# Performance work log

Measured on AMD Instinct MI355X. Metric: run time of the kernel, lower is better.

## Reference

```python
import jax, jax.numpy as jnp
import numpy as np

WS = 7          # window size
NH = 8          # num heads
EPS = 1e-5


def _rel_pos_index(ws):
    # timm WindowAttention relative_position_index, shape (ws*ws, ws*ws), values in [0, (2ws-1)^2)
    coords = np.stack(np.meshgrid(np.arange(ws), np.arange(ws), indexing='ij'))  # 2,ws,ws
    coords = coords.reshape(2, -1)
    rel = coords[:, :, None] - coords[:, None, :]          # 2,N,N
    rel = rel.transpose(1, 2, 0)                           # N,N,2
    rel[:, :, 0] += ws - 1
    rel[:, :, 1] += ws - 1
    rel[:, :, 0] *= 2 * ws - 1
    return rel.sum(-1)                                     # N,N

RPI = jnp.asarray(_rel_pos_index(WS), dtype=jnp.int32)


def _ln(x, g, b):
    mu = jnp.mean(x, axis=-1, keepdims=True)
    var = jnp.mean(jnp.square(x - mu), axis=-1, keepdims=True)
    return (x - mu) * jax.lax.rsqrt(var + EPS) * g + b


def setup_inputs() -> dict:
    key = jax.random.key(0)
    ks = jax.random.split(key, 16)
    C, Hd, V = 256, 1024, 7
    s = lambda k, shp, fan: jax.random.normal(k, shp, jnp.float32) * (fan ** -0.5)
    return {
        'x': jax.random.normal(ks[0], (256, 256, 14, 14), jnp.float32),
        'conv_w': s(ks[1], (C, C), C), 'conv_b': jnp.zeros((C,), jnp.float32),
        'ln1_g': jnp.ones((C,), jnp.float32), 'ln1_b': jnp.zeros((C,), jnp.float32),
        'qkv_w': s(ks[2], (C, 3 * C), C), 'qkv_b': jnp.zeros((3 * C,), jnp.float32),
        'rpb': 0.02 * jax.random.normal(ks[3], ((2 * WS - 1) ** 2, NH), jnp.float32),
        'proj_w': s(ks[4], (C, C), C), 'proj_b': jnp.zeros((C,), jnp.float32),
        'ln2_g': jnp.ones((C,), jnp.float32), 'ln2_b': jnp.zeros((C,), jnp.float32),
        'fc1_w': s(ks[5], (C, Hd), C), 'fc1_b': jnp.zeros((Hd,), jnp.float32),
        'fc2_w': s(ks[6], (Hd, C), Hd), 'fc2_b': jnp.zeros((C,), jnp.float32),
        'fc_out_w': s(ks[7], (C, V), C), 'fc_out_b': jnp.zeros((V,), jnp.float32),
    }


def reference(x, conv_w, conv_b, ln1_g, ln1_b, qkv_w, qkv_b, rpb, proj_w, proj_b,
              ln2_g, ln2_b, fc1_w, fc1_b, fc2_w, fc2_b, fc_out_w, fc_out_b):
    B, Cin, H, W = x.shape
    C = conv_w.shape[0]
    hd = C // NH
    # 1x1 conv projection -> tokens (B, H*W, C)
    t = jnp.einsum('oc,bchw->bhwo', conv_w, x) + conv_b            # B,H,W,C
    tok = t.reshape(B, H * W, C)
    # --- Swin block, shift_size=0 ---
    shortcut = tok
    y = _ln(tok, ln1_g, ln1_b).reshape(B, H, W, C)
    # window partition -> (B*nW, ws*ws, C)
    nHw, nWw = H // WS, W // WS
    yw = y.reshape(B, nHw, WS, nWw, WS, C).transpose(0, 1, 3, 2, 4, 5)
    yw = yw.reshape(B * nHw * nWw, WS * WS, C)
    N = WS * WS
    qkv = (yw @ qkv_w + qkv_b).reshape(-1, N, 3, NH, hd).transpose(2, 0, 3, 1, 4)
    q, k, v = qkv[0], qkv[1], qkv[2]                               # (Bn, NH, N, hd)
    attn = jnp.einsum('bhqd,bhkd->bhqk', q * (hd ** -0.5), k)
    attn = attn + rpb[RPI].transpose(2, 0, 1)[None]                # + (NH,N,N) bias
    attn = jax.nn.softmax(attn, axis=-1)
    o = jnp.einsum('bhqk,bhkd->bqhd', attn, v).reshape(-1, N, C)
    o = o @ proj_w + proj_b
    # window reverse
    o = o.reshape(B, nHw, nWw, WS, WS, C).transpose(0, 1, 3, 2, 4, 5).reshape(B, H * W, C)
    tok = shortcut + o                                             # drop_path = identity (eval)
    h = _ln(tok, ln2_g, ln2_b)
    h = jax.nn.gelu(h @ fc1_w + fc1_b, approximate=False) @ fc2_w + fc2_b
    tok = tok + h
    # global average pool over spatial tokens, then classifier
    pooled = jnp.mean(tok, axis=1)                                 # B,C
    return pooled @ fc_out_w + fc_out_b
```

## Files before the change

kernel.cpp:

```cpp
#include <hip/hip_runtime.h>
#include <math.h>

#define NHEADS 8
#define BATCH  256
#define HWTOK  196
#define MTOT   50176

#define BM 128
#define BN 128
#define BK 64

typedef short bfrag8 __attribute__((ext_vector_type(8)));
typedef float ffrag4 __attribute__((ext_vector_type(4)));

__device__ __forceinline__ unsigned short f2bf(float f) {
  union { float f; unsigned u; } v; v.f = f;
  unsigned r = v.u + 0x7fffu + ((v.u >> 16) & 1u);
  return (unsigned short)(r >> 16);
}
__device__ __forceinline__ float bf2f(unsigned short b) {
  union { unsigned u; float f; } v; v.u = ((unsigned)b) << 16;
  return v.f;
}
__device__ __forceinline__ float bflo(unsigned u) {
  union { unsigned x; float f; } v; v.x = u << 16; return v.f;
}
__device__ __forceinline__ float bfhi(unsigned u) {
  union { unsigned x; float f; } v; v.x = u & 0xffff0000u; return v.f;
}
__device__ __forceinline__ unsigned cvtpk(float a, float b) {
  unsigned r;
  asm("v_cvt_pk_bf16_f32 %0, %1, %2" : "=v"(r) : "v"(a), "v"(b));
  return r;
}
__device__ __forceinline__ float gelu_fast(float x) {
  float ax = fabsf(x);
  float z = ax * 0.70710678118654752f;
  float t = __builtin_amdgcn_rcpf(fmaf(z, 0.3275911f, 1.0f));
  float y = t * (0.254829592f +
            t * (-0.284496736f +
            t * (1.421413741f +
            t * (-1.453152027f +
            t * 1.061405429f))));
  float e2 = __expf(-z * z);
  float erfv = fmaf(-y, e2, 1.0f);
  return 0.5f * fmaf(ax, erfv, x);
}
__device__ __forceinline__ int window_reverse_row(int m) {
  int widx = m / 49, pos = m % 49;
  int b = widx >> 2, wh = (widx >> 1) & 1, ww = widx & 1;
  int i = pos / 7, j = pos % 7;
  return b * 196 + (wh * 7 + i) * 14 + (ww * 7 + j);
}

__device__ __forceinline__ void gload16(const void* g, void* l) {
  __builtin_amdgcn_global_load_lds(
      (const __attribute__((address_space(1))) void*)g,
      (__attribute__((address_space(3))) void*)l, 16, 0, 0);
}

__device__ __forceinline__ int xcd_swz() {
  if (gridDim.x & 7) return (int)blockIdx.x;
  return (int)((blockIdx.x & 7) * (gridDim.x >> 3) + (blockIdx.x >> 3));
}

template <int EPI>
__global__ __launch_bounds__(256) void k_gemm_mfma(const unsigned short* __restrict__ A,
                                                   const unsigned short* __restrict__ BT,
                                                   const float* __restrict__ bias,
                                                   void* __restrict__ Cout,
                                                   int rowbase, int N, int K, int nNt) {
  __shared__ __align__(128) unsigned short S[16384];
  const int t = threadIdx.x;
  const int lane = t & 63, w = t >> 6;
  const int wr = w >> 1, wc = w & 1;
  const int lb = xcd_swz();
  const int n_t = lb % nNt, m_t = lb / nNt;
  const int m0 = m_t * BM, n0 = n_t * BN;
  const int l15 = lane & 15;
  const int sw = (lane & 7) << 3;
  const int rA = lane >> 3;
  const int kin = (((lane & 7) ^ rA) << 3);
  ffrag4 acc[4][4] = {};

  for (int k0 = 0; k0 < K; k0 += BK) {
#pragma unroll
    for (int i = 0; i < 4; ++i) {
      const int seg = i * 4 + w;
      const int row = seg * 8 + rA;
      gload16(A + (size_t)(m0 + row) * K + k0 + kin, (char*)S + seg * 1024);
      gload16(BT + (size_t)(n0 + row) * K + k0 + kin, (char*)S + 16384 + seg * 1024);
    }
    __syncthreads();
#pragma unroll
    for (int kk = 0; kk < BK; kk += 32) {
      bfrag8 af[4], bfr[4];
      const int colA = (kk + (lane >> 4) * 8) ^ sw;
#pragma unroll
      for (int mi = 0; mi < 4; ++mi) {
        int row = wr * 64 + mi * 16 + l15;
        af[mi] = *(const bfrag8*)&S[row * BK + colA];
      }
#pragma unroll
      for (int ni = 0; ni < 4; ++ni) {
        int col = wc * 64 + ni * 16 + l15;
        bfr[ni] = *(const bfrag8*)&S[8192 + col * BK + colA];
      }
#pragma unroll
      for (int mi = 0; mi < 4; ++mi)
#pragma unroll
        for (int ni = 0; ni < 4; ++ni)
          acc[mi][ni] = __builtin_amdgcn_mfma_f32_16x16x32_bf16(af[mi], bfr[ni], acc[mi][ni], 0, 0, 0);
    }
    __syncthreads();
  }

  const int cr = (lane >> 4) * 4;
  const int cc = l15;
  float bv[4];
#pragma unroll
  for (int ni = 0; ni < 4; ++ni) bv[ni] = bias[n0 + wc * 64 + ni * 16 + cc];

  float* Sf = (float*)S;
#pragma unroll
  for (int pass = 0; pass < 2; ++pass) {
    if (wr == pass) {
#pragma unroll
      for (int mi = 0; mi < 4; ++mi) {
#pragma unroll
        for (int j = 0; j < 4; ++j) {
          const int mloc = mi * 16 + cr + j;
#pragma unroll
          for (int ni = 0; ni < 4; ++ni) {
            const int nl = wc * 64 + ni * 16 + cc;
            Sf[mloc * 128 + nl] = acc[mi][ni][j] + bv[ni];
          }
        }
      }
    }
    __syncthreads();
#pragma unroll
    for (int r = 0; r < 4; ++r) {
      const int flat = (r * 256 + t) * 8;
      const int ml = flat >> 7, nl = flat & 127;
      float4 a = *(const float4*)&Sf[flat];
      float4 b2 = *(const float4*)&Sf[flat + 4];
      uint4 o;
      if (EPI == 2 || EPI == 3) {
        const int gm = rowbase + m0 + pass * 64 + ml;
        const int row = (EPI == 2) ? window_reverse_row(gm) : gm;
        unsigned short* dst = (unsigned short*)Cout + (size_t)row * N + n0 + nl;
        uint4 old = *(const uint4*)dst;
        o.x = cvtpk(bflo(old.x) + a.x, bfhi(old.x) + a.y);
        o.y = cvtpk(bflo(old.y) + a.z, bfhi(old.y) + a.w);
        o.z = cvtpk(bflo(old.z) + b2.x, bfhi(old.z) + b2.y);
        o.w = cvtpk(bflo(old.w) + b2.z, bfhi(old.w) + b2.w);
        *(uint4*)dst = o;
      } else {
        o.x = cvtpk(a.x, a.y);  o.y = cvtpk(a.z, a.w);
        o.z = cvtpk(b2.x, b2.y); o.w = cvtpk(b2.z, b2.w);
        *(uint4*)((unsigned short*)Cout + (size_t)(m0 + pass * 64 + ml) * N + n0 + nl) = o;
      }
    }
    if (pass == 0) __syncthreads();
  }
}

__global__ __launch_bounds__(256, 1) void k_mlp(const unsigned short* __restrict__ A,
                                                const unsigned short* __restrict__ fc1T,
                                                const unsigned short* __restrict__ fc2T,
                                                const float* __restrict__ b1g,
                                                const float* __restrict__ b2g,
                                                unsigned short* __restrict__ tok,
                                                int rowbase) {
  __shared__ __align__(128) char S[131072];
  unsigned short* Al = (unsigned short*)S;
  unsigned short* Bl = (unsigned short*)(S + 65536);
  unsigned short* Cl = (unsigned short*)(S + 98304);

  const int t = threadIdx.x;
  const int lane = t & 63, w = t >> 6;
  const int wr = w >> 1, wc = w & 1;
  const int l15 = lane & 15, g = lane >> 4;
  const int key = lane & 7;
  const int cr = (lane >> 4) * 4, cc = l15;
  const int m0 = xcd_swz() * 128;

  ffrag4 acc2[4][8] = {};

#pragma unroll
  for (int i = 0; i < 16; ++i) {
    const int inst = i * 4 + w;
    const int r = inst * 2 + (lane >> 5);
    const int sg = ((lane & 31) ^ (r & 7)) << 3;
    gload16(A + (size_t)(m0 + r) * 256 + sg, (char*)Al + inst * 1024);
  }

  for (int hc = 0; hc < 8; ++hc) {
    float b1[4];
#pragma unroll
    for (int ni = 0; ni < 4; ++ni)
      b1[ni] = b1g[hc * 128 + wc * 64 + ni * 16 + cc];

    ffrag4 acch[4][4] = {};
#pragma unroll
    for (int p = 0; p < 2; ++p) {
      __syncthreads();
#pragma unroll
      for (int i = 0; i < 8; ++i) {
        const int inst = i * 4 + w;
        const int r = inst * 4 + (lane >> 4);
        const int sg = p * 128 + (((lane & 15) ^ (r & 7)) << 3);
        gload16(fc1T + (size_t)(hc * 128 + r) * 256 + sg, (char*)Bl + inst * 1024);
      }
      __syncthreads();
#pragma unroll
      for (int kk = 0; kk < 128; kk += 32) {
        bfrag8 af[4], bf[4];
        const int qA = ((p * 16 + (kk >> 3) + g) ^ key) << 3;
        const int qB = (((kk >> 3) + g) ^ key) << 3;
#pragma unroll
        for (int mi = 0; mi < 4; ++mi)
          af[mi] = *(const bfrag8*)&Al[(wr * 64 + mi * 16 + l15) * 256 + qA];
#pragma unroll
        for (int ni = 0; ni < 4; ++ni)
          bf[ni] = *(const bfrag8*)&Bl[(wc * 64 + ni * 16 + l15) * 128 + qB];
#pragma unroll
        for (int mi = 0; mi < 4; ++mi)
#pragma unroll
          for (int ni = 0; ni < 4; ++ni)
            acch[mi][ni] = __builtin_amdgcn_mfma_f32_16x16x32_bf16(af[mi], bf[ni], acch[mi][ni], 0, 0, 0);
      }
    }
    __syncthreads();

#pragma unroll
    for (int mi = 0; mi < 4; ++mi) {
#pragma unroll
      for (int j = 0; j < 4; ++j) {
        const int row = wr * 64 + mi * 16 + cr + j;
        const int k8 = (row & 7) << 3;
#pragma unroll
        for (int ni = 0; ni < 4; ++ni) {
          const int col = wc * 64 + ni * 16 + cc;
          Cl[row * 128 + (col ^ k8)] = f2bf(gelu_fast(acch[mi][ni][j] + b1[ni]));
        }
      }
    }

#pragma unroll
    for (int h = 0; h < 2; ++h) {
      if (h == 1) __syncthreads();
#pragma unroll
      for (int i = 0; i < 8; ++i) {
        const int inst = i * 4 + w;
        const int r = inst * 8 + (lane >> 3);
        const int sg = hc * 128 + h * 64 + (((lane & 7) ^ (r & 7)) << 3);
        gload16(fc2T + (size_t)r * 1024 + sg, (char*)Bl + inst * 1024);
      }
      __syncthreads();
#pragma unroll
      for (int kk2 = 0; kk2 < 64; kk2 += 32) {
        bfrag8 af2[4], bf2[8];
        const int qC = ((h * 8 + (kk2 >> 3) + g) ^ key) << 3;
        const int qB2 = (((kk2 >> 3) + g) ^ key) << 3;
#pragma unroll
        for (int mi = 0; mi < 4; ++mi)
          af2[mi] = *(const bfrag8*)&Cl[(wr * 64 + mi * 16 + l15) * 128 + qC];
#pragma unroll
        for (int ni = 0; ni < 8; ++ni)
          bf2[ni] = *(const bfrag8*)&Bl[(wc * 128 + ni * 16 + l15) * 64 + qB2];
#pragma unroll
        for (int mi = 0; mi < 4; ++mi)
#pragma unroll
          for (int ni = 0; ni < 8; ++ni)
            acc2[mi][ni] = __builtin_amdgcn_mfma_f32_16x16x32_bf16(af2[mi], bf2[ni], acc2[mi][ni], 0, 0, 0);
      }
    }
  }

  __syncthreads();
  float b2v[8];
#pragma unroll
  for (int ni = 0; ni < 8; ++ni) b2v[ni] = b2g[wc * 128 + ni * 16 + cc];

  float* Sf = (float*)S;
#pragma unroll
  for (int pass = 0; pass < 2; ++pass) {
    if (wr == pass) {
#pragma unroll
      for (int mi = 0; mi < 4; ++mi) {
#pragma unroll
        for (int j = 0; j < 4; ++j) {
          const int mloc = mi * 16 + cr + j;
#pragma unroll
          for (int ni = 0; ni < 8; ++ni) {
            const int nl = wc * 128 + ni * 16 + cc;
            Sf[mloc * 256 + nl] = acc2[mi][ni][j] + b2v[ni];
          }
        }
      }
    }
    __syncthreads();
#pragma unroll
    for (int r = 0; r < 8; ++r) {
      const int flat = (r * 256 + t) * 8;
      const int ml = flat >> 8, nl = flat & 255;
      float4 a = *(const float4*)&Sf[flat];
      float4 b = *(const float4*)&Sf[flat + 4];
      const int gm = rowbase + m0 + pass * 64 + ml;
      unsigned short* dst = tok + (size_t)gm * 256 + nl;
      uint4 old = *(const uint4*)dst;
      uint4 o;
      o.x = cvtpk(bflo(old.x) + a.x, bfhi(old.x) + a.y);
      o.y = cvtpk(bflo(old.y) + a.z, bfhi(old.y) + a.w);
      o.z = cvtpk(bflo(old.z) + b.x, bfhi(old.z) + b.y);
      o.w = cvtpk(bflo(old.w) + b.z, bfhi(old.w) + b.w);
      *(uint4*)dst = o;
    }
    if (pass == 0) __syncthreads();
  }
}

__global__ __launch_bounds__(256) void k_wtrans(const float* __restrict__ w,
                                                unsigned short* __restrict__ wt,
                                                int K, int N) {
  __shared__ float tile[32][33];
  int k0 = blockIdx.x * 32, n0 = blockIdx.y * 32;
  int tx = threadIdx.x & 31, ty = threadIdx.x >> 5;
#pragma unroll
  for (int r = 0; r < 4; ++r)
    tile[ty + r * 8][tx] = w[(size_t)(k0 + ty + r * 8) * N + n0 + tx];
  __syncthreads();
#pragma unroll
  for (int r = 0; r < 4; ++r)
    wt[(size_t)(n0 + ty + r * 8) * K + k0 + tx] = f2bf(tile[tx][ty + r * 8]);
}

__global__ __launch_bounds__(256) void k_cast(const float* __restrict__ w,
                                              unsigned short* __restrict__ wb, int n) {
  int i = blockIdx.x * 256 + threadIdx.x;
  if (i < n) wb[i] = f2bf(w[i]);
}

__global__ __launch_bounds__(256) void k_transpose_x(const float* __restrict__ x,
                                                     unsigned short* __restrict__ xt) {
  __shared__ float tile[32][33];
  int b = blockIdx.x;
  int hw0 = blockIdx.y * 32;
  int c0 = blockIdx.z * 32;
  int tx = threadIdx.x & 31, ty = threadIdx.x >> 5;
#pragma unroll
  for (int r = 0; r < 4; ++r) {
    int c = c0 + ty + r * 8, hw = hw0 + tx;
    if (hw < HWTOK) tile[ty + r * 8][tx] = x[((size_t)b * 256 + c) * HWTOK + hw];
  }
  __syncthreads();
#pragma unroll
  for (int r = 0; r < 4; ++r) {
    int hw = hw0 + ty + r * 8, c = c0 + tx;
    if (hw < HWTOK) xt[((size_t)b * HWTOK + hw) * 256 + c] = f2bf(tile[tx][ty + r * 8]);
  }
}

template <bool WINDOW>
__global__ __launch_bounds__(256) void k_layernorm(const unsigned short* __restrict__ in,
                                                   const float* __restrict__ g,
                                                   const float* __restrict__ bta,
                                                   unsigned short* __restrict__ out,
                                                   int rowbase) {
  int wid = threadIdx.x >> 6, lane = threadIdx.x & 63;
  int li = blockIdx.x * 4 + wid;
  int token = rowbase + li;
  const uint2 xr = *(const uint2*)(in + (size_t)token * 256 + lane * 4);
  float x0 = bflo(xr.x), x1 = bfhi(xr.x), x2 = bflo(xr.y), x3 = bfhi(xr.y);
  float s = x0 + x1 + x2 + x3;
  float sq = x0 * x0 + x1 * x1 + x2 * x2 + x3 * x3;
#pragma unroll
  for (int off = 32; off >= 1; off >>= 1) {
    s += __shfl_xor(s, off);
    sq += __shfl_xor(sq, off);
  }
  float mean = s * (1.f / 256.f);
  float var = sq * (1.f / 256.f) - mean * mean;
  float rstd = rsqrtf(var + 1e-5f);
  float4 gv = *(const float4*)(g + lane * 4);
  float4 bv = *(const float4*)(bta + lane * 4);
  uint2 ov;
  ov.x = cvtpk((x0 - mean) * rstd * gv.x + bv.x,
               (x1 - mean) * rstd * gv.y + bv.y);
  ov.y = cvtpk((x2 - mean) * rstd * gv.z + bv.z,
               (x3 - mean) * rstd * gv.w + bv.w);
  int orow;
  if (WINDOW) {
    int b = token / 196, hw = token % 196;
    int h14 = hw / 14, w14 = hw % 14;
    int wh = h14 / 7, i = h14 % 7, ww = w14 / 7, j = w14 % 7;
    int widx = (b * 2 + wh) * 2 + ww;
    orow = widx * 49 + i * 7 + j - rowbase;
  } else {
    orow = li;
  }
  *(uint2*)(out + (size_t)orow * 256 + lane * 4) = ov;
}

__global__ __launch_bounds__(256) void k_attention(const unsigned short* __restrict__ qkv,
                                                   const float* __restrict__ rpb,
                                                   unsigned short* __restrict__ o) {
  __shared__ unsigned short Kl[4][64 * 40];
  __shared__ unsigned short VTl[4][32 * 72];
  __shared__ unsigned short Pl[4][64 * 72];
  __shared__ float rpbl[4][176];

  const int t = threadIdx.x;
  const int w4 = t >> 6, lane = t & 63;
  const int l15 = lane & 15, g = lane >> 4;
  const int gw = blockIdx.x * 4 + w4;
  const int lw = gw >> 3, head = gw & 7;

  unsigned short* K_ = Kl[w4];
  unsigned short* VT_ = VTl[w4];
  unsigned short* P_ = Pl[w4];
  float* rpb_ = rpbl[w4];

  const size_t baseq = (size_t)lw * 49 * 768 + head * 32;

  for (int e = lane; e < 169; e += 64) rpb_[e] = rpb[e * 8 + head];

  for (int e = lane; e < 512; e += 64) {
    int d = e >> 4, tk = 48 + (e & 15);
    if ((e & 15) != 0) VT_[d * 72 + tk] = 0;
  }

  for (int e = lane; e < 784; e += 64) {
    int tok = e >> 4, dp = e & 15;
    unsigned kv = *(const unsigned*)(qkv + baseq + 256 + (size_t)tok * 768 + dp * 2);
    *(unsigned*)&K_[tok * 40 + dp * 2] = kv;
    unsigned vv = *(const unsigned*)(qkv + baseq + 512 + (size_t)tok * 768 + dp * 2);
    VT_[(dp * 2 + 0) * 72 + tok] = (unsigned short)(vv & 0xffffu);
    VT_[(dp * 2 + 1) * 72 + tok] = (unsigned short)(vv >> 16);
  }

  ffrag4 acc[4][4] = {};
  {
    bfrag8 af[4], bfr[4];
#pragma unroll
    for (int qi = 0; qi < 4; ++qi)
      af[qi] = *(const bfrag8*)(qkv + baseq + (size_t)(16 * qi + l15) * 768 + g * 8);
#pragma unroll
    for (int kj = 0; kj < 4; ++kj)
      bfr[kj] = *(const bfrag8*)&K_[(16 * kj + l15) * 40 + g * 8];
#pragma unroll
    for (int qi = 0; qi < 4; ++qi)
#pragma unroll
      for (int kj = 0; kj < 4; ++kj)
        acc[qi][kj] = __builtin_amdgcn_mfma_f32_16x16x32_bf16(af[qi], bfr[kj], acc[qi][kj], 0, 0, 0);
  }

  const float scale = 0.17677669529663687f;
  int kc[4];
  bool kvalid[4];
#pragma unroll
  for (int kj = 0; kj < 4; ++kj) {
    int c = 16 * kj + l15;
    kc[kj] = 13 * (c / 7) + (c % 7);
    kvalid[kj] = (c < 49);
  }
#pragma unroll
  for (int qi = 0; qi < 4; ++qi) {
#pragma unroll
    for (int j = 0; j < 4; ++j) {
      int q = 16 * qi + 4 * g + j;
      int qc = 13 * (q / 7) + (q % 7);
      float tv[4];
#pragma unroll
      for (int kj = 0; kj < 4; ++kj)
        tv[kj] = kvalid[kj] ? (acc[qi][kj][j] * scale + rpb_[qc - kc[kj] + 84]) : -INFINITY;
      float mx = fmaxf(fmaxf(tv[0], tv[1]), fmaxf(tv[2], tv[3]));
#pragma unroll
      for (int off = 8; off >= 1; off >>= 1) mx = fmaxf(mx, __shfl_xor(mx, off));
      float p[4], sum = 0.f;
#pragma unroll
      for (int kj = 0; kj < 4; ++kj) {
        p[kj] = kvalid[kj] ? __expf(tv[kj] - mx) : 0.f;
        sum += p[kj];
      }
#pragma unroll
      for (int off = 8; off >= 1; off >>= 1) sum += __shfl_xor(sum, off);
      float inv = __builtin_amdgcn_rcpf(sum);
      if (q < 49) {
#pragma unroll
        for (int kj = 0; kj < 4; ++kj)
          P_[q * 72 + 16 * kj + l15] = f2bf(p[kj] * inv);
      }
    }
  }

  ffrag4 accO[2][4] = {};
#pragma unroll
  for (int kk = 0; kk < 64; kk += 32) {
    bfrag8 af2[2], bf2[4];
#pragma unroll
    for (int ti = 0; ti < 2; ++ti)
      af2[ti] = *(const bfrag8*)&VT_[(16 * ti + l15) * 72 + kk + g * 8];
#pragma unroll
    for (int qj = 0; qj < 4; ++qj)
      bf2[qj] = *(const bfrag8*)&P_[(16 * qj + l15) * 72 + kk + g * 8];
#pragma unroll
    for (int ti = 0; ti < 2; ++ti)
#pragma unroll
      for (int qj = 0; qj < 4; ++qj)
        accO[ti][qj] = __builtin_amdgcn_mfma_f32_16x16x32_bf16(af2[ti], bf2[qj], accO[ti][qj], 0, 0, 0);
  }

#pragma unroll
  for (int qj = 0; qj < 4; ++qj) {
    int q = 16 * qj + l15;
    if (q < 49) {
#pragma unroll
      for (int ti = 0; ti < 2; ++ti) {
        uint2 ov;
        ov.x = cvtpk(accO[ti][qj][0], accO[ti][qj][1]);
        ov.y = cvtpk(accO[ti][qj][2], accO[ti][qj][3]);
        *(uint2*)(o + ((size_t)lw * 49 + q) * 256 + head * 32 + 16 * ti + 4 * g) = ov;
      }
    }
  }
}

__global__ __launch_bounds__(256) void k_pool(const unsigned short* __restrict__ tok,
                                              float* __restrict__ pooled) {
  int b = blockIdx.x, c = threadIdx.x;
  float s = 0.f;
  for (int hw = 0; hw < 196; ++hw) s += bf2f(tok[((size_t)b * 196 + hw) * 256 + c]);
  pooled[b * 256 + c] = s * (1.f / 196.f);
}

__global__ __launch_bounds__(64) void k_head(const float* __restrict__ pooled,
                                             const float* __restrict__ w,
                                             const float* __restrict__ bias,
                                             float* __restrict__ out) {
  int b = blockIdx.x, t = threadIdx.x;
  if (t < 7) {
    float s = bias[t];
    for (int c = 0; c < 256; ++c) s = fmaf(pooled[b * 256 + c], w[c * 7 + t], s);
    out[b * 7 + t] = s;
  }
}

extern "C" void kernel_launch(void* const* d_in, const int* in_sizes, int n_in,
                              void* d_out, int out_size, void* d_ws, size_t ws_size,
                              hipStream_t stream) {
  const float* x      = (const float*)d_in[0];
  const float* conv_w = (const float*)d_in[1];
  const float* conv_b = (const float*)d_in[2];
  const float* ln1_g  = (const float*)d_in[3];
  const float* ln1_b  = (const float*)d_in[4];
  const float* qkv_w  = (const float*)d_in[5];
  const float* qkv_b  = (const float*)d_in[6];
  const float* rpb    = (const float*)d_in[7];
  const float* proj_w = (const float*)d_in[8];
  const float* proj_b = (const float*)d_in[9];
  const float* ln2_g  = (const float*)d_in[10];
  const float* ln2_b  = (const float*)d_in[11];
  const float* fc1_w  = (const float*)d_in[12];
  const float* fc1_b  = (const float*)d_in[13];
  const float* fc2_w  = (const float*)d_in[14];
  const float* fc2_b  = (const float*)d_in[15];
  const float* fco_w  = (const float*)d_in[16];
  const float* fco_b  = (const float*)d_in[17];
  float* out = (float*)d_out;
  char* p = (char*)d_ws;

  const size_t FULL_NEED = 182000000ull;
  const int nch = (ws_size >= FULL_NEED) ? 1 : 4;
  const int chw = 1024 / nch;
  const size_t chrows = (size_t)chw * 49;
  const int nMt = (int)(chrows / BM);

  unsigned short* tok = (unsigned short*)p;   p += (size_t)MTOT * 256 * 2;
  unsigned short* Bbuf = (unsigned short*)p;  p += chrows * 1024 * 2;
  unsigned short* Abuf = (unsigned short*)p;  p += chrows * 256 * 2;
  unsigned short* Cbuf = (unsigned short*)p;  p += chrows * 256 * 2;
  unsigned short* cwB  = (unsigned short*)p;  p += 65536 * 2;
  unsigned short* qkvT = (unsigned short*)p;  p += 196608 * 2;
  unsigned short* projT= (unsigned short*)p;  p += 65536 * 2;
  unsigned short* fc1T = (unsigned short*)p;  p += 262144 * 2;
  unsigned short* fc2T = (unsigned short*)p;  p += 262144 * 2;
  float* pool = (float*)p;                    p += 65536 * 4;
  unsigned short* xt = Bbuf;

  k_cast<<<256, 256, 0, stream>>>(conv_w, cwB, 65536);
  k_wtrans<<<dim3(8, 24), 256, 0, stream>>>(qkv_w, qkvT, 256, 768);
  k_wtrans<<<dim3(8, 8), 256, 0, stream>>>(proj_w, projT, 256, 256);
  k_wtrans<<<dim3(8, 32), 256, 0, stream>>>(fc1_w, fc1T, 256, 1024);
  k_wtrans<<<dim3(32, 8), 256, 0, stream>>>(fc2_w, fc2T, 1024, 256);

  k_transpose_x<<<dim3(BATCH, 7, 8), 256, 0, stream>>>(x, xt);
  k_gemm_mfma<0><<<(MTOT / BM) * 2, 256, 0, stream>>>(xt, cwB, conv_b, tok, 0, 256, 256, 2);

  for (int c = 0; c < nch; ++c) {
    const int rowbase = c * (int)chrows;
    k_layernorm<true><<<chrows / 4, 256, 0, stream>>>(tok, ln1_g, ln1_b, Abuf, rowbase);
    k_gemm_mfma<0><<<nMt * 6, 256, 0, stream>>>(Abuf, qkvT, qkv_b, Bbuf, 0, 768, 256, 6);
    k_attention<<<chw * 2, 256, 0, stream>>>(Bbuf, rpb, Cbuf);
    k_gemm_mfma<2><<<nMt * 2, 256, 0, stream>>>(Cbuf, projT, proj_b, tok, rowbase, 256, 256, 2);
    k_layernorm<false><<<chrows / 4, 256, 0, stream>>>(tok, ln2_g, ln2_b, Abuf, rowbase);
    k_mlp<<<nMt, 256, 0, stream>>>(Abuf, fc1T, fc2T, fc1_b, fc2_b, tok, rowbase);
  }

  k_pool<<<BATCH, 256, 0, stream>>>(tok, pool);
  k_head<<<BATCH, 64, 0, stream>>>(pool, fco_w, fco_b, out);
}
```

Before: 337.5 us.

## Shrink fused MLP shared memory to 64KB for two blocks per CU

The fused MLP kernel stops keeping the whole 128x256 activation tile resident in LDS. It now streams A and fc1 in K-chunks of 64 through a 32KB staging area, which halves shared memory to 64KB and raises launch bounds to allow two blocks per CU. The cost is reloading the A tile from global memory for each of the 8 hidden chunks, more barriers, and tighter register limits that could cause spills with the 4x8 accumulator array. A GELU option is also added to the generic GEMM epilogue for EPI==1.

After: 468.5 us. 38.8% more time.

```diff
diff --git a/kernel.cpp b/kernel.cpp
--- a/kernel.cpp
+++ b/kernel.cpp
@@ -133,7 +133,9 @@
 #pragma unroll
           for (int ni = 0; ni < 4; ++ni) {
             const int nl = wc * 64 + ni * 16 + cc;
-            Sf[mloc * 128 + nl] = acc[mi][ni][j] + bv[ni];
+            float v = acc[mi][ni][j] + bv[ni];
+            if (EPI == 1) v = gelu_fast(v);
+            Sf[mloc * 128 + nl] = v;
           }
         }
       }
@@ -166,36 +168,29 @@
   }
 }
 
-__global__ __launch_bounds__(256, 1) void k_mlp(const unsigned short* __restrict__ A,
+__global__ __launch_bounds__(256, 2) void k_mlp(const unsigned short* __restrict__ A,
                                                 const unsigned short* __restrict__ fc1T,
                                                 const unsigned short* __restrict__ fc2T,
                                                 const float* __restrict__ b1g,
                                                 const float* __restrict__ b2g,
                                                 unsigned short* __restrict__ tok,
                                                 int rowbase) {
-  __shared__ __align__(128) char S[131072];
-  unsigned short* Al = (unsigned short*)S;
-  unsigned short* Bl = (unsigned short*)(S + 65536);
-  unsigned short* Cl = (unsigned short*)(S + 98304);
+  __shared__ __align__(128) char S[65536];
+  unsigned short* Ss = (unsigned short*)S;
+  unsigned short* Cl = (unsigned short*)(S + 32768);
 
   const int t = threadIdx.x;
   const int lane = t & 63, w = t >> 6;
   const int wr = w >> 1, wc = w & 1;
   const int l15 = lane & 15, g = lane >> 4;
-  const int key = lane & 7;
+  const int sw = (lane & 7) << 3;
+  const int rA = lane >> 3;
+  const int kin = (((lane & 7) ^ rA) << 3);
   const int cr = (lane >> 4) * 4, cc = l15;
   const int m0 = xcd_swz() * 128;
 
   ffrag4 acc2[4][8] = {};
 
-#pragma unroll
-  for (int i = 0; i < 16; ++i) {
-    const int inst = i * 4 + w;
-    const int r = inst * 2 + (lane >> 5);
-    const int sg = ((lane & 31) ^ (r & 7)) << 3;
-    gload16(A + (size_t)(m0 + r) * 256 + sg, (char*)Al + inst * 1024);
-  }
-
   for (int hc = 0; hc < 8; ++hc) {
     float b1[4];
 #pragma unroll
@@ -203,36 +198,34 @@
       b1[ni] = b1g[hc * 128 + wc * 64 + ni * 16 + cc];
 
     ffrag4 acch[4][4] = {};
-#pragma unroll
-    for (int p = 0; p < 2; ++p) {
+    for (int k0 = 0; k0 < 256; k0 += 64) {
+#pragma unroll
+      for (int i = 0; i < 4; ++i) {
+        const int seg = i * 4 + w;
+        const int row = seg * 8 + rA;
+        gload16(A + (size_t)(m0 + row) * 256 + k0 + kin, (char*)S + seg * 1024);
+        gload16(fc1T + (size_t)(hc * 128 + row) * 256 + k0 + kin,
+                (char*)S + 16384 + seg * 1024);
+      }
       __syncthreads();
 #pragma unroll
-      for (int i = 0; i < 8; ++i) {
-        const int inst = i * 4 + w;
-        const int r = inst * 4 + (lane >> 4);
-        const int sg = p * 128 + (((lane & 15) ^ (r & 7)) << 3);
-        gload16(fc1T + (size_t)(hc * 128 + r) * 256 + sg, (char*)Bl + inst * 1024);
-      }
-      __syncthreads();
-#pragma unroll
-      for (int kk = 0; kk < 128; kk += 32) {
+      for (int kk = 0; kk < 64; kk += 32) {
         bfrag8 af[4], bf[4];
-        const int qA = ((p * 16 + (kk >> 3) + g) ^ key) << 3;
-        const int qB = (((kk >> 3) + g) ^ key) << 3;
+        const int colA = (kk + g * 8) ^ sw;
 #pragma unroll
         for (int mi = 0; mi < 4; ++mi)
-          af[mi] = *(const bfrag8*)&Al[(wr * 64 + mi * 16 + l15) * 256 + qA];
+          af[mi] = *(const bfrag8*)&Ss[(wr * 64 + mi * 16 + l15) * 64 + colA];
 #pragma unroll
         for (int ni = 0; ni < 4; ++ni)
-          bf[ni] = *(const bfrag8*)&Bl[(wc * 64 + ni * 16 + l15) * 128 + qB];
+          bf[ni] = *(const bfrag8*)&Ss[8192 + (wc * 64 + ni * 16 + l15) * 64 + colA];
 #pragma unroll
         for (int mi = 0; mi < 4; ++mi)
 #pragma unroll
           for (int ni = 0; ni < 4; ++ni)
             acch[mi][ni] = __builtin_amdgcn_mfma_f32_16x16x32_bf16(af[mi], bf[ni], acch[mi][ni], 0, 0, 0);
       }
-    }
-    __syncthreads();
+      __syncthreads();
+    }
 
 #pragma unroll
     for (int mi = 0; mi < 4; ++mi) {
@@ -250,36 +243,35 @@
 
 #pragma unroll
     for (int h = 0; h < 2; ++h) {
-      if (h == 1) __syncthreads();
 #pragma unroll
       for (int i = 0; i < 8; ++i) {
         const int inst = i * 4 + w;
         const int r = inst * 8 + (lane >> 3);
         const int sg = hc * 128 + h * 64 + (((lane & 7) ^ (r & 7)) << 3);
-        gload16(fc2T + (size_t)r * 1024 + sg, (char*)Bl + inst * 1024);
+        gload16(fc2T + (size_t)r * 1024 + sg, (char*)S + inst * 1024);
       }
       __syncthreads();
 #pragma unroll
       for (int kk2 = 0; kk2 < 64; kk2 += 32) {
         bfrag8 af2[4], bf2[8];
-        const int qC = ((h * 8 + (kk2 >> 3) + g) ^ key) << 3;
-        const int qB2 = (((kk2 >> 3) + g) ^ key) << 3;
+        const int qC = ((h * 8 + (kk2 >> 3) + g) ^ (lane & 7)) << 3;
+        const int qB = (((kk2 >> 3) + g) ^ (lane & 7)) << 3;
 #pragma unroll
         for (int mi = 0; mi < 4; ++mi)
           af2[mi] = *(const bfrag8*)&Cl[(wr * 64 + mi * 16 + l15) * 128 + qC];
 #pragma unroll
         for (int ni = 0; ni < 8; ++ni)
-          bf2[ni] = *(const bfrag8*)&Bl[(wc * 128 + ni * 16 + l15) * 64 + qB2];
+          bf2[ni] = *(const bfrag8*)&Ss[(wc * 128 + ni * 16 + l15) * 64 + qB];
 #pragma unroll
         for (int mi = 0; mi < 4; ++mi)
 #pragma unroll
           for (int ni = 0; ni < 8; ++ni)
             acc2[mi][ni] = __builtin_amdgcn_mfma_f32_16x16x32_bf16(af2[mi], bf2[ni], acc2[mi][ni], 0, 0, 0);
       }
-    }
-  }
-
-  __syncthreads();
+      __syncthreads();
+    }
+  }
+
   float b2v[8];
 #pragma unroll
   for (int ni = 0; ni < 8; ++ni) b2v[ni] = b2g[wc * 128 + ni * 16 + cc];
```
